# Kernel tuning notes

Measured on AMD Instinct MI355X. Metric: run time of the kernel, lower is better.

## Reference

```python
import jax, jax.numpy as jnp
import numpy as np

N_NODES = 100000
N_EDGES = 1600000
IN_CH, HID, OUT_CH = 128, 64, 16


def setup_inputs() -> dict:
    key = jax.random.key(0)
    k1, k2, k3, k4 = jax.random.split(key, 4)
    x = jax.random.normal(k1, (N_NODES, IN_CH), dtype=jnp.float32)
    edge_index = jax.random.randint(k2, (2, N_EDGES), 0, N_NODES, dtype=jnp.int64)
    # glorot-style scaled weights, zero bias (PyG GCNConv default)
    W1 = jax.random.normal(k3, (IN_CH, HID), dtype=jnp.float32) * (1.0 / np.sqrt(IN_CH))
    b1 = jnp.zeros((HID,), dtype=jnp.float32)
    W2 = jax.random.normal(k4, (HID, OUT_CH), dtype=jnp.float32) * (1.0 / np.sqrt(HID))
    b2 = jnp.zeros((OUT_CH,), dtype=jnp.float32)
    return {"x": x, "edge_index": edge_index, "W1": W1, "b1": b1, "W2": W2, "b2": b2}


def _gcn_conv(x, src, dst, W, b, n_nodes):
    """PyG GCNConv: linear transform, then sym-normalized scatter-add aggregation.
    src/dst already include self-loops."""
    xl = x @ W  # [N, out]
    deg = jax.ops.segment_sum(jnp.ones_like(dst, dtype=xl.dtype), dst, num_segments=n_nodes)
    dinv = jnp.where(deg > 0, jax.lax.rsqrt(deg), 0.0)  # deg^-1/2 (inf -> 0)
    norm = dinv[src] * dinv[dst]  # [E]
    msg = xl[src] * norm[:, None]  # gather + scale, [E, out]
    out = jax.ops.segment_sum(msg, dst, num_segments=n_nodes)  # scatter-add
    return out + b


def reference(x, edge_index, W1, b1, W2, b2):
    n = x.shape[0]
    loops = jnp.arange(n, dtype=edge_index.dtype)
    src = jnp.concatenate([edge_index[0], loops])  # add self-loops
    dst = jnp.concatenate([edge_index[1], loops])
    h = jax.nn.relu(_gcn_conv(x, src, dst, W1, b1, n))
    out = _gcn_conv(h, src, dst, W2, b2, n)
    return out
```

## Files before the change

### kernel.cpp

```cpp
#include <hip/hip_runtime.h>
#include <hip/hip_bf16.h>

#define IN_CH 128
#define HID 64
#define OUT_CH 16

#define G_SH 7
#define G_SZ 128
#define NBK_MAX 800
#define CHUNK 4096
#define CAP 4096

#define XROW 136

typedef short bf16x8 __attribute__((ext_vector_type(8)));
typedef float f32x4 __attribute__((ext_vector_type(4)));

__device__ __forceinline__ float bf_lo(unsigned w) { return __uint_as_float(w << 16); }
__device__ __forceinline__ float bf_hi(unsigned w) { return __uint_as_float(w & 0xffff0000u); }

__device__ __forceinline__ unsigned short f2bf(float f) {
    __hip_bfloat16 h = __float2bfloat16(f);
    unsigned short u;
    __builtin_memcpy(&u, &h, 2);
    return u;
}

__device__ __forceinline__ unsigned pack_bf2(float lo, float hi) {
    return ((unsigned)f2bf(hi) << 16) | (unsigned)f2bf(lo);
}


__global__ void k_init_bcur(int* __restrict__ p, int nb) {
    int i = blockIdx.x * blockDim.x + threadIdx.x;
    if (i < nb) p[i] = i * CAP;
}


__global__ void k_cvtW(const float* __restrict__ W, unsigned short* __restrict__ wt) {
    int i = blockIdx.x * blockDim.x + threadIdx.x;
    if (i < IN_CH * HID) {
        int ch = i >> 7, k = i & 127;
        wt[ch * IN_CH + k] = f2bf(W[k * HID + ch]);
    }
}

__global__ __launch_bounds__(256) void k_bucket(const int* __restrict__ ei,
                                                int* __restrict__ bcursor,
                                                int* __restrict__ packed, int E, int nb) {
    __shared__ int hcnt[NBK_MAX];
    __shared__ int hoff[NBK_MAX];
    __shared__ int hbase[NBK_MAX];
    __shared__ int hcur[NBK_MAX];
    __shared__ int stage[CHUNK];
    __shared__ unsigned short sbk[CHUNK];
    __shared__ int scan_s[256];
    __shared__ int sh_carry;

    int tid = threadIdx.x;
    int base = blockIdx.x * CHUNK;
    int cnt = E - base;
    if (cnt > CHUNK) cnt = CHUNK;
    for (int t = tid; t < nb; t += 256) { hcnt[t] = 0; hcur[t] = 0; }
    if (tid == 0) sh_carry = 0;
    __syncthreads();

    int mp[CHUNK / 256], mb[CHUNK / 256];
#pragma unroll
    for (int k = 0; k < CHUNK / 256; ++k) {
        int idx = base + k * 256 + tid;
        int p = 0, b = -1;
        if (idx < E) {
            int s = ei[idx];
            int d = ei[E + idx];
            b = d >> G_SH;
            p = ((d & (G_SZ - 1)) << 17) | s;
            atomicAdd(&hcnt[b], 1);
        }
        mp[k] = p; mb[k] = b;
    }
    __syncthreads();

    for (int s0 = 0; s0 < nb; s0 += 256) {
        int i = s0 + tid;
        int v = (i < nb) ? hcnt[i] : 0;
        scan_s[tid] = v;
        __syncthreads();
        for (int off = 1; off < 256; off <<= 1) {
            int t = (tid >= off) ? scan_s[tid - off] : 0;
            __syncthreads();
            scan_s[tid] += t;
            __syncthreads();
        }
        if (i < nb) hoff[i] = sh_carry + scan_s[tid] - v;
        __syncthreads();
        if (tid == 255) sh_carry += scan_s[255];
        __syncthreads();
    }

    for (int t = tid; t < nb; t += 256)
        if (hcnt[t] > 0) hbase[t] = atomicAdd(&bcursor[t], hcnt[t]);
    __syncthreads();

#pragma unroll
    for (int k = 0; k < CHUNK / 256; ++k) {
        int b = mb[k];
        if (b >= 0) {
            int slot = hoff[b] + atomicAdd(&hcur[b], 1);
            stage[slot] = mp[k];
            sbk[slot] = (unsigned short)b;
        }
    }
    __syncthreads();

    for (int i = tid; i < cnt; i += 256) {
        int b = sbk[i];
        packed[hbase[b] + (i - hoff[b])] = stage[i];
    }
}


__global__ __launch_bounds__(256) void k_sortbkt(const int* __restrict__ bcursor,
                                                 int* __restrict__ packed,
                                                 int* __restrict__ rowptr,
                                                 int* __restrict__ counts,
                                                 float* __restrict__ dinv, int n) {
    __shared__ int sc[G_SZ];
    __shared__ int lcur[G_SZ];
    __shared__ int stage[CAP];
    __shared__ int sorted_[CAP];

    int tid = threadIdx.x;
    int bkt = blockIdx.x;
    int d0 = bkt << G_SH;
    int base = bkt * CAP;
    int L = bcursor[bkt] - base;

    if (tid < G_SZ) sc[tid] = 0;
    __syncthreads();
    for (int i = tid; i < L; i += 256) {
        int p = packed[base + i];
        stage[i] = p;
        atomicAdd(&sc[p >> 17], 1);
    }
    __syncthreads();
    int v = (tid < G_SZ) ? sc[tid] : 0;
    for (int off = 1; off < G_SZ; off <<= 1) {
        int t = (tid < G_SZ && tid >= off) ? sc[tid - off] : 0;
        __syncthreads();
        if (tid < G_SZ) sc[tid] += t;
        __syncthreads();
    }
    if (tid < G_SZ) {
        int excl = sc[tid] - v;
        lcur[tid] = excl;
        int d = d0 + tid;
        if (d < n) {
            rowptr[d] = base + excl;
            counts[d] = v;
            dinv[d] = rsqrtf((float)(v + 1));
        }
    }
    __syncthreads();
    for (int i = tid; i < L; i += 256) {
        int p = stage[i];
        int pos = atomicAdd(&lcur[p >> 17], 1);
        sorted_[pos] = p & 0x1FFFF;
    }
    __syncthreads();
    for (int i = tid; i < L; i += 256) packed[base + i] = sorted_[i];
}


__global__ __launch_bounds__(256) void k_gemm1(const float* __restrict__ x,
                                               const unsigned short* __restrict__ wt,
                                               const float* __restrict__ dinv,
                                               __hip_bfloat16* __restrict__ xlp, int n) {
    __shared__ unsigned short sx[64 * XROW];
    __shared__ unsigned short sw[64 * XROW];
    int tid = threadIdx.x;
    int node0 = blockIdx.x * 64;

    for (int i = tid; i < 64 * 16; i += 256) {
        int row = i >> 4, kk = i & 15;
        uint4 v = ((const uint4*)wt)[i];
        *(uint4*)&sw[row * XROW + kk * 8] = v;
    }
    for (int i = tid; i < 64 * 32; i += 256) {
        int row = i >> 5, k4 = i & 31;
        int node = node0 + row;
        float4 v = (node < n) ? ((const float4*)(x + (size_t)node * IN_CH))[k4]
                              : make_float4(0.f, 0.f, 0.f, 0.f);
        uint2 p;
        p.x = pack_bf2(v.x, v.y);
        p.y = pack_bf2(v.z, v.w);
        *(uint2*)&sx[row * XROW + k4 * 4] = p;
    }
    __syncthreads();

    int w = tid >> 6, lane = tid & 63;
    int lrow = lane & 15, lg = lane >> 4;
    f32x4 acc0 = {0.f, 0.f, 0.f, 0.f}, acc1 = {0.f, 0.f, 0.f, 0.f};
    f32x4 acc2 = {0.f, 0.f, 0.f, 0.f}, acc3 = {0.f, 0.f, 0.f, 0.f};
    const unsigned short* ax = &sx[(16 * w + lrow) * XROW + lg * 8];
#pragma unroll
    for (int k0 = 0; k0 < IN_CH; k0 += 32) {
        bf16x8 a = *(const bf16x8*)&ax[k0];
        bf16x8 b0 = *(const bf16x8*)&sw[(lrow) * XROW + lg * 8 + k0];
        bf16x8 b1 = *(const bf16x8*)&sw[(16 + lrow) * XROW + lg * 8 + k0];
        bf16x8 b2 = *(const bf16x8*)&sw[(32 + lrow) * XROW + lg * 8 + k0];
        bf16x8 b3 = *(const bf16x8*)&sw[(48 + lrow) * XROW + lg * 8 + k0];
        acc0 = __builtin_amdgcn_mfma_f32_16x16x32_bf16(a, b0, acc0, 0, 0, 0);
        acc1 = __builtin_amdgcn_mfma_f32_16x16x32_bf16(a, b1, acc1, 0, 0, 0);
        acc2 = __builtin_amdgcn_mfma_f32_16x16x32_bf16(a, b2, acc2, 0, 0, 0);
        acc3 = __builtin_amdgcn_mfma_f32_16x16x32_bf16(a, b3, acc3, 0, 0, 0);
    }
#pragma unroll
    for (int r = 0; r < 4; ++r) {
        int node = node0 + 16 * w + lg * 4 + r;
        if (node < n) {
            float dd = dinv[node];
            __hip_bfloat16* o = xlp + (size_t)node * HID + lrow;
            o[0]  = __float2bfloat16(dd * acc0[r]);
            o[16] = __float2bfloat16(dd * acc1[r]);
            o[32] = __float2bfloat16(dd * acc2[r]);
            o[48] = __float2bfloat16(dd * acc3[r]);
        }
    }
}

__global__ __launch_bounds__(256) void k_agg1(const int* __restrict__ rowptr,
                                              const int* __restrict__ counts,
                                              const int* __restrict__ esrc,
                                              const float* __restrict__ dinv,
                                              const __hip_bfloat16* __restrict__ xlp,
                                              const float* __restrict__ b,
                                              float* __restrict__ hout, int n) {
    int d = blockIdx.x * 8 + (threadIdx.x >> 5);
    if (d >= n) return;
    int cl = threadIdx.x & 31;
    int j0 = rowptr[d];
    int cnt = counts[d];
    float a0 = 0.f, a1 = 0.f;
    int t = 0;
    for (; t + 8 <= cnt; t += 8) {
        int s0 = esrc[j0 + t],     s1 = esrc[j0 + t + 1];
        int s2 = esrc[j0 + t + 2], s3 = esrc[j0 + t + 3];
        int s4 = esrc[j0 + t + 4], s5 = esrc[j0 + t + 5];
        int s6 = esrc[j0 + t + 6], s7 = esrc[j0 + t + 7];
        unsigned w0 = ((const unsigned*)(xlp + (size_t)s0 * HID))[cl];
        unsigned w1 = ((const unsigned*)(xlp + (size_t)s1 * HID))[cl];
        unsigned w2 = ((const unsigned*)(xlp + (size_t)s2 * HID))[cl];
        unsigned w3 = ((const unsigned*)(xlp + (size_t)s3 * HID))[cl];
        unsigned w4 = ((const unsigned*)(xlp + (size_t)s4 * HID))[cl];
        unsigned w5 = ((const unsigned*)(xlp + (size_t)s5 * HID))[cl];
        unsigned w6 = ((const unsigned*)(xlp + (size_t)s6 * HID))[cl];
        unsigned w7 = ((const unsigned*)(xlp + (size_t)s7 * HID))[cl];
        a0 += ((bf_lo(w0) + bf_lo(w1)) + (bf_lo(w2) + bf_lo(w3))) +
              ((bf_lo(w4) + bf_lo(w5)) + (bf_lo(w6) + bf_lo(w7)));
        a1 += ((bf_hi(w0) + bf_hi(w1)) + (bf_hi(w2) + bf_hi(w3))) +
              ((bf_hi(w4) + bf_hi(w5)) + (bf_hi(w6) + bf_hi(w7)));
    }
    for (; t + 4 <= cnt; t += 4) {
        int s0 = esrc[j0 + t],     s1 = esrc[j0 + t + 1];
        int s2 = esrc[j0 + t + 2], s3 = esrc[j0 + t + 3];
        unsigned w0 = ((const unsigned*)(xlp + (size_t)s0 * HID))[cl];
        unsigned w1 = ((const unsigned*)(xlp + (size_t)s1 * HID))[cl];
        unsigned w2 = ((const unsigned*)(xlp + (size_t)s2 * HID))[cl];
        unsigned w3 = ((const unsigned*)(xlp + (size_t)s3 * HID))[cl];
        a0 += (bf_lo(w0) + bf_lo(w1)) + (bf_lo(w2) + bf_lo(w3));
        a1 += (bf_hi(w0) + bf_hi(w1)) + (bf_hi(w2) + bf_hi(w3));
    }
    for (; t < cnt; ++t) {
        int s = esrc[j0 + t];
        unsigned w = ((const unsigned*)(xlp + (size_t)s * HID))[cl];
        a0 += bf_lo(w);
        a1 += bf_hi(w);
    }
    unsigned ws = ((const unsigned*)(xlp + (size_t)d * HID))[cl];
    float dd = dinv[d];
    float v0 = dd * (a0 + bf_lo(ws)) + b[2 * cl];
    float v1 = dd * (a1 + bf_hi(ws)) + b[2 * cl + 1];
    ((float2*)(hout + (size_t)d * HID))[cl] = make_float2(fmaxf(v0, 0.f), fmaxf(v1, 0.f));
}


__global__ __launch_bounds__(256) void k_gemm2(const float* __restrict__ h,
                                               const float* __restrict__ W,
                                               const float* __restrict__ dinv,
                                               __hip_bfloat16* __restrict__ hlp, int n) {
    __shared__ float sW[HID * OUT_CH];
    __shared__ float sh[16][HID];
    int tid = threadIdx.x;
    for (int t = tid; t < HID * OUT_CH; t += 256) sW[t] = W[t];
    int node0 = blockIdx.x * 16;
    for (int t = tid; t < 16 * HID / 4; t += 256) {
        int r = t >> 4, k4 = t & 15;
        int node = node0 + r;
        float4 v = (node < n) ? ((const float4*)(h + (size_t)node * HID))[k4]
                              : make_float4(0.f, 0.f, 0.f, 0.f);
        ((float4*)sh[r])[k4] = v;
    }
    __syncthreads();
    int r = tid >> 4, j = tid & 15;
    int node = node0 + r;
    if (node >= n) return;
    float acc = 0.f;
#pragma unroll
    for (int k = 0; k < HID; ++k)
        acc += sh[r][k] * sW[k * OUT_CH + j];
    hlp[(size_t)node * OUT_CH + j] = __float2bfloat16(dinv[node] * acc);
}

__global__ __launch_bounds__(256) void k_agg2(const int* __restrict__ rowptr,
                                              const int* __restrict__ counts,
                                              const int* __restrict__ esrc,
                                              const float* __restrict__ dinv,
                                              const __hip_bfloat16* __restrict__ hlp,
                                              const float* __restrict__ b,
                                              float* __restrict__ out, int n) {
    int d = blockIdx.x * 32 + (threadIdx.x >> 3);
    if (d >= n) return;
    int cl = threadIdx.x & 7;
    int j0 = rowptr[d];
    int cnt = counts[d];
    float a0 = 0.f, a1 = 0.f;
    int t = 0;
    for (; t + 8 <= cnt; t += 8) {
        int s0 = esrc[j0 + t],     s1 = esrc[j0 + t + 1];
        int s2 = esrc[j0 + t + 2], s3 = esrc[j0 + t + 3];
        int s4 = esrc[j0 + t + 4], s5 = esrc[j0 + t + 5];
        int s6 = esrc[j0 + t + 6], s7 = esrc[j0 + t + 7];
        unsigned w0 = ((const unsigned*)(hlp + (size_t)s0 * OUT_CH))[cl];
        unsigned w1 = ((const unsigned*)(hlp + (size_t)s1 * OUT_CH))[cl];
        unsigned w2 = ((const unsigned*)(hlp + (size_t)s2 * OUT_CH))[cl];
        unsigned w3 = ((const unsigned*)(hlp + (size_t)s3 * OUT_CH))[cl];
        unsigned w4 = ((const unsigned*)(hlp + (size_t)s4 * OUT_CH))[cl];
        unsigned w5 = ((const unsigned*)(hlp + (size_t)s5 * OUT_CH))[cl];
        unsigned w6 = ((const unsigned*)(hlp + (size_t)s6 * OUT_CH))[cl];
        unsigned w7 = ((const unsigned*)(hlp + (size_t)s7 * OUT_CH))[cl];
        a0 += ((bf_lo(w0) + bf_lo(w1)) + (bf_lo(w2) + bf_lo(w3))) +
              ((bf_lo(w4) + bf_lo(w5)) + (bf_lo(w6) + bf_lo(w7)));
        a1 += ((bf_hi(w0) + bf_hi(w1)) + (bf_hi(w2) + bf_hi(w3))) +
              ((bf_hi(w4) + bf_hi(w5)) + (bf_hi(w6) + bf_hi(w7)));
    }
    for (; t + 4 <= cnt; t += 4) {
        int s0 = esrc[j0 + t],     s1 = esrc[j0 + t + 1];
        int s2 = esrc[j0 + t + 2], s3 = esrc[j0 + t + 3];
        unsigned w0 = ((const unsigned*)(hlp + (size_t)s0 * OUT_CH))[cl];
        unsigned w1 = ((const unsigned*)(hlp + (size_t)s1 * OUT_CH))[cl];
        unsigned w2 = ((const unsigned*)(hlp + (size_t)s2 * OUT_CH))[cl];
        unsigned w3 = ((const unsigned*)(hlp + (size_t)s3 * OUT_CH))[cl];
        a0 += (bf_lo(w0) + bf_lo(w1)) + (bf_lo(w2) + bf_lo(w3));
        a1 += (bf_hi(w0) + bf_hi(w1)) + (bf_hi(w2) + bf_hi(w3));
    }
    for (; t < cnt; ++t) {
        int s = esrc[j0 + t];
        unsigned w = ((const unsigned*)(hlp + (size_t)s * OUT_CH))[cl];
        a0 += bf_lo(w);
        a1 += bf_hi(w);
    }
    unsigned ws = ((const unsigned*)(hlp + (size_t)d * OUT_CH))[cl];
    float dd = dinv[d];
    float v0 = dd * (a0 + bf_lo(ws)) + b[2 * cl];
    float v1 = dd * (a1 + bf_hi(ws)) + b[2 * cl + 1];
    ((float2*)(out + (size_t)d * OUT_CH))[cl] = make_float2(v0, v1);
}

extern "C" void kernel_launch(void* const* d_in, const int* in_sizes, int n_in,
                              void* d_out, int out_size, void* d_ws, size_t ws_size,
                              hipStream_t stream) {
    const float* x  = (const float*)d_in[0];
    const int* ei   = (const int*)d_in[1];
    const float* W1 = (const float*)d_in[2];
    const float* b1 = (const float*)d_in[3];
    const float* W2 = (const float*)d_in[4];
    const float* b2 = (const float*)d_in[5];
    float* out = (float*)d_out;

    const int n = in_sizes[0] / IN_CH;
    const int E = in_sizes[1] / 2;
    const int nb = (n + G_SZ - 1) >> G_SH;
    const int nchunk = (E + CHUNK - 1) / CHUNK;

    int* rowptr  = (int*)d_ws;
    int* counts  = rowptr + n;
    int* bcursor = counts + n;
    unsigned short* wtbf = (unsigned short*)(bcursor + 1024);
    int* packed  = (int*)(wtbf + 8192);
    float* dinv  = (float*)(packed + (size_t)nb * CAP);
    __hip_bfloat16* xlp = (__hip_bfloat16*)(dinv + n);
    __hip_bfloat16* hlp = xlp;
    float* hout  = (float*)(xlp + (size_t)n * HID);

    k_init_bcur<<<(nb + 255) / 256, 256, 0, stream>>>(bcursor, nb);
    k_cvtW<<<(IN_CH * HID + 255) / 256, 256, 0, stream>>>(W1, wtbf);
    k_bucket<<<nchunk, 256, 0, stream>>>(ei, bcursor, packed, E, nb);
    k_sortbkt<<<nb, 256, 0, stream>>>(bcursor, packed, rowptr, counts, dinv, n);

    k_gemm1<<<(n + 63) / 64, 256, 0, stream>>>(x, wtbf, dinv, xlp, n);
    k_agg1<<<(n + 7) / 8, 256, 0, stream>>>(rowptr, counts, packed, dinv, xlp, b1, hout, n);

    k_gemm2<<<(n + 15) / 16, 256, 0, stream>>>(hout, W2, dinv, hlp, n);
    k_agg2<<<(n + 31) / 32, 256, 0, stream>>>(rowptr, counts, packed, dinv, hlp, b2, out, n);
}
```

Before: 131.7 us.

## Fuse second-layer linear transform into first aggregation kernel

Merges k_agg1 and k_gemm2 into a single kernel. Each 32-lane group aggregates one node's hidden row, applies bias and ReLU, stages it in shared memory, and multiplies it by W2 held in LDS using a two-half split reduced with a shuffle. This removes the fp32 hidden-activation round trip through global memory and one kernel launch. In exchange, every block reloads W2 into LDS and adds a block-wide barrier after the irregular gather loop.

```diff
diff --git a/kernel.cpp b/kernel.cpp
--- a/kernel.cpp
+++ b/kernel.cpp
@@ -229,18 +229,29 @@
     }
 }
 
-__global__ __launch_bounds__(256) void k_agg1(const int* __restrict__ rowptr,
-                                              const int* __restrict__ counts,
-                                              const int* __restrict__ esrc,
-                                              const float* __restrict__ dinv,
-                                              const __hip_bfloat16* __restrict__ xlp,
-                                              const float* __restrict__ b,
-                                              float* __restrict__ hout, int n) {
-    int d = blockIdx.x * 8 + (threadIdx.x >> 5);
-    if (d >= n) return;
-    int cl = threadIdx.x & 31;
-    int j0 = rowptr[d];
-    int cnt = counts[d];
+
+__global__ __launch_bounds__(256) void k_agg1f(const int* __restrict__ rowptr,
+                                               const int* __restrict__ counts,
+                                               const int* __restrict__ esrc,
+                                               const float* __restrict__ dinv,
+                                               const __hip_bfloat16* __restrict__ xlp,
+                                               const float* __restrict__ b1,
+                                               const float* __restrict__ W2,
+                                               __hip_bfloat16* __restrict__ hlp, int n) {
+    __shared__ float sW2[HID * OUT_CH];
+    __shared__ float sh[8][HID];
+    int tid = threadIdx.x;
+    for (int i = tid; i < HID * OUT_CH; i += 256) sW2[i] = W2[i];
+    __syncthreads();
+
+    int g = tid >> 5;
+    int cl = tid & 31;
+    int d = blockIdx.x * 8 + g;
+    bool active = (d < n);
+    int j0 = 0, cnt = 0;
+    float dd = 0.f;
+    if (active) { j0 = rowptr[d]; cnt = counts[d]; dd = dinv[d]; }
+
     float a0 = 0.f, a1 = 0.f;
     int t = 0;
     for (; t + 8 <= cnt; t += 8) {
@@ -277,40 +288,29 @@
         a0 += bf_lo(w);
         a1 += bf_hi(w);
     }
-    unsigned ws = ((const unsigned*)(xlp + (size_t)d * HID))[cl];
-    float dd = dinv[d];
-    float v0 = dd * (a0 + bf_lo(ws)) + b[2 * cl];
-    float v1 = dd * (a1 + bf_hi(ws)) + b[2 * cl + 1];
-    ((float2*)(hout + (size_t)d * HID))[cl] = make_float2(fmaxf(v0, 0.f), fmaxf(v1, 0.f));
-}
-
-
-__global__ __launch_bounds__(256) void k_gemm2(const float* __restrict__ h,
-                                               const float* __restrict__ W,
-                                               const float* __restrict__ dinv,
-                                               __hip_bfloat16* __restrict__ hlp, int n) {
-    __shared__ float sW[HID * OUT_CH];
-    __shared__ float sh[16][HID];
-    int tid = threadIdx.x;
-    for (int t = tid; t < HID * OUT_CH; t += 256) sW[t] = W[t];
-    int node0 = blockIdx.x * 16;
-    for (int t = tid; t < 16 * HID / 4; t += 256) {
-        int r = t >> 4, k4 = t & 15;
-        int node = node0 + r;
-        float4 v = (node < n) ? ((const float4*)(h + (size_t)node * HID))[k4]
-                              : make_float4(0.f, 0.f, 0.f, 0.f);
-        ((float4*)sh[r])[k4] = v;
-    }
-    __syncthreads();
-    int r = tid >> 4, j = tid & 15;
-    int node = node0 + r;
-    if (node >= n) return;
-    float acc = 0.f;
-#pragma unroll
-    for (int k = 0; k < HID; ++k)
-        acc += sh[r][k] * sW[k * OUT_CH + j];
-    hlp[(size_t)node * OUT_CH + j] = __float2bfloat16(dinv[node] * acc);
-}
+
+    if (active) {
+        unsigned ws = ((const unsigned*)(xlp + (size_t)d * HID))[cl];
+        float v0 = fmaxf(dd * (a0 + bf_lo(ws)) + b1[2 * cl], 0.f);
+        float v1 = fmaxf(dd * (a1 + bf_hi(ws)) + b1[2 * cl + 1], 0.f);
+        ((float2*)sh[g])[cl] = make_float2(v0, v1);
+    }
+    __syncthreads();
+
+    if (active) {
+        int j = cl & 15, kh = cl >> 4;
+        float acc = 0.f;
+#pragma unroll 8
+        for (int k = 0; k < 32; ++k) {
+            int kk = kh * 32 + k;
+            acc += sh[g][kk] * sW2[kk * OUT_CH + j];
+        }
+        acc += __shfl_xor(acc, 16);
+        if (cl < 16)
+            hlp[(size_t)d * OUT_CH + j] = __float2bfloat16(dd * acc);
+    }
+}
+
 
 __global__ __launch_bounds__(256) void k_agg2(const int* __restrict__ rowptr,
                                               const int* __restrict__ counts,
@@ -390,8 +390,7 @@
     int* packed  = (int*)(wtbf + 8192);
     float* dinv  = (float*)(packed + (size_t)nb * CAP);
     __hip_bfloat16* xlp = (__hip_bfloat16*)(dinv + n);
-    __hip_bfloat16* hlp = xlp;
-    float* hout  = (float*)(xlp + (size_t)n * HID);
+    __hip_bfloat16* hlp = xlp + (size_t)n * HID;
 
     k_init_bcur<<<(nb + 255) / 256, 256, 0, stream>>>(bcursor, nb);
     k_cvtW<<<(IN_CH * HID + 255) / 256, 256, 0, stream>>>(W1, wtbf);
@@ -399,8 +398,7 @@
     k_sortbkt<<<nb, 256, 0, stream>>>(bcursor, packed, rowptr, counts, dinv, n);
 
     k_gemm1<<<(n + 63) / 64, 256, 0, stream>>>(x, wtbf, dinv, xlp, n);
-    k_agg1<<<(n + 7) / 8, 256, 0, stream>>>(rowptr, counts, packed, dinv, xlp, b1, hout, n);
-
-    k_gemm2<<<(n + 15) / 16, 256, 0, stream>>>(hout, W2, dinv, hlp, n);
+    k_agg1f<<<(n + 7) / 8, 256, 0, stream>>>(rowptr, counts, packed, dinv, xlp, b1, W2, hlp, n);
+
     k_agg2<<<(n + 31) / 32, 256, 0, stream>>>(rowptr, counts, packed, dinv, hlp, b2, out, n);
 }
```

Result: faster. 128.2 us (-2.6%).
